# Kernel optimization log

Hardware: AMD Instinct MI355X
Metric: run time of the kernel (lower is better)

The kernel has to match this reference:

```python
import jax, jax.numpy as jnp
import numpy as np

B, M, Wc, K, IN = 32, 65536, 64, 8, 512
R = K + 1                      # sparse_reads + last_used slot
IFACE = 2 * Wc + R + 1         # interface_size = 2w + r + 1


def setup_inputs() -> dict:
    key = jax.random.key(0)
    ks = jax.random.split(key, 8)
    xi = jax.random.normal(ks[0], (B, IN), jnp.float32)
    sparse = jax.random.normal(ks[1], (B, M, Wc), jnp.float32)
    read_weights = jax.random.uniform(ks[2], (B, 1, R), jnp.float32)
    read_vectors = jax.random.normal(ks[3], (B, R, Wc), jnp.float32)
    W = jax.random.normal(ks[4], (IN, IFACE), jnp.float32) / np.sqrt(IN).astype(np.float32)
    b = jnp.zeros((IFACE,), jnp.float32)
    read_positions = jax.random.randint(ks[5], (B, R), 0, M, dtype=jnp.int32)
    last_used_mem = jax.random.randint(ks[6], (B,), 0, M, dtype=jnp.int32)
    return dict(xi=xi, sparse=sparse, read_weights=read_weights,
                read_vectors=read_vectors, W=W, b=b,
                read_positions=read_positions, last_used_mem=last_used_mem)


def reference(xi, sparse, read_weights, read_vectors, W, b, read_positions, last_used_mem):
    bsz = xi.shape[0]
    w, r, m, k = Wc, R, M, K
    # interface linear (independent_linears=False path)
    iface = xi @ W + b                                   # [b, 2w+r+1]
    read_query = iface[:, :w]                            # [b, w]
    write_vector = iface[:, w:2 * w][:, None, :]         # [b, 1, w]
    ig = iface[:, 2 * w:2 * w + r][:, None, :]           # [b, 1, r]
    write_gate = jax.nn.sigmoid(iface[:, -1])[:, None, None]  # [b, 1, 1]
    # write(): interpolate read weights, rank-1 update of read_vectors
    ww = write_gate * (ig * read_weights + (1.0 - ig))   # [b, 1, r]
    rv = read_vectors + jnp.einsum('bor,bow->brw', ww, write_vector)  # [b, r, w]
    # write_into_memory(): for l in range(b): sparse[:, positions[l], :] = rv
    flat_pos = read_positions.reshape(-1)                # [b*r]
    flat_k = jnp.tile(jnp.arange(r, dtype=jnp.int32), bsz)
    order = jnp.full((m,), -1, jnp.int32).at[flat_pos].max(
        jnp.arange(bsz * r, dtype=jnp.int32))            # last writer per slot
    k_final = flat_k[order[flat_pos]]                    # winning k per written entry
    sparse = sparse.at[:, flat_pos, :].set(rv[:, k_final, :])
    # read_from_sparse_memory(): brute-force exact KNN (squared L2, replaces FLANN kd-tree)
    d = (jnp.sum(sparse * sparse, -1)
         - 2.0 * jnp.einsum('bmw,bw->bm', sparse, read_query)
         + jnp.sum(read_query * read_query, -1, keepdims=True))  # [b, m]
    neg_d, pos = jax.lax.top_k(-d, k)                    # k nearest
    dist = -neg_d                                        # [b, k]
    pos = jnp.concatenate([pos.astype(jnp.int32), last_used_mem[:, None]], axis=1)  # [b, r]
    dist = jnp.concatenate([dist, jnp.zeros((bsz, 1), dist.dtype)], axis=1)          # [b, r]
    dist = dist / jnp.max(dist, axis=1, keepdims=True)   # distances / max(distances)
    gathered = jnp.take_along_axis(sparse, pos[:, :, None], axis=1)  # [b, r, w]
    read_weights_new = dist[:, None, :]                  # [b, 1, r]
    return gathered[:, :k, :], read_weights_new, gathered
```

## Files before the change

### kernel.cpp

```cpp
#include <hip/hip_runtime.h>
#include <float.h>
#include <math.h>

#define Bz    32
#define Mz    65536
#define WCz   64
#define Rz    9
#define INz   512
#define IFz   138
#define NBLK  64
#define RPB   1024


__device__ __forceinline__ bool pless(float d1, int i1, float d2, int i2) {
    return (d1 < d2) || (d1 == d2 && i1 < i2);
}

__global__ __launch_bounds__(256) void k_iface(
    const float* __restrict__ xi, const float* __restrict__ W,
    const float* __restrict__ bias, float* __restrict__ iface)
{
    int o = blockIdx.x * 256 + threadIdx.x;
    if (o >= Bz * IFz) return;
    int b = o / IFz, j = o % IFz;
    const float* x = xi + b * INz;
    float a0 = 0.f, a1 = 0.f, a2 = 0.f, a3 = 0.f;
    #pragma unroll 4
    for (int i = 0; i < INz; i += 4) {
        a0 = fmaf(x[i + 0], W[(i + 0) * IFz + j], a0);
        a1 = fmaf(x[i + 1], W[(i + 1) * IFz + j], a1);
        a2 = fmaf(x[i + 2], W[(i + 2) * IFz + j], a2);
        a3 = fmaf(x[i + 3], W[(i + 3) * IFz + j], a3);
    }
    iface[o] = (a0 + a1) + (a2 + a3) + bias[j];
}

__global__ __launch_bounds__(256) void k_prep(
    const float* __restrict__ iface,
    const float* __restrict__ read_weights,
    const float* __restrict__ read_vectors,
    const int*   __restrict__ read_positions,
    float* __restrict__ ws_q, float* __restrict__ ws_qq,
    float* __restrict__ ws_rv, float* __restrict__ ws_dv,
    int* __restrict__ ws_wpos, int* __restrict__ ws_wk, int* __restrict__ ws_nw)
{
    __shared__ float ww_s[Bz * Rz];
    __shared__ int nw_s;
    int t = threadIdx.x;
    if (t == 0) nw_s = 0;

    for (int i = t; i < Bz * WCz; i += 256) {
        int b = i >> 6, w = i & 63;
        ws_q[i] = iface[b * IFz + w];
    }
    for (int i = t; i < Bz * Rz; i += 256) {
        int b = i / Rz, r = i % Rz;
        float x    = iface[b * IFz + (IFz - 1)];
        float gate = 1.0f / (1.0f + expf(-x));
        float ig   = iface[b * IFz + 2 * WCz + r];
        float rw   = read_weights[i];
        ww_s[i] = gate * (ig * rw + (1.0f - ig));
    }
    __syncthreads();

    if (t < Bz) {
        float s = 0.f;
        for (int w = 0; w < WCz; w++) { float v = ws_q[t * WCz + w]; s = fmaf(v, v, s); }
        ws_qq[t] = s;
    }
    for (int i = t; i < Bz * Rz * WCz; i += 256) {
        int br = i >> 6, w = i & 63;
        int b  = br / Rz;
        ws_rv[i] = fmaf(ww_s[br], iface[b * IFz + WCz + w], read_vectors[i]);
    }
    for (int i = t; i < Bz * Rz; i += 256) {
        int p = read_positions[i];
        bool win = true;
        for (int j = i + 1; j < Bz * Rz; j++)
            if (read_positions[j] == p) { win = false; break; }
        if (win) {
            int slot = atomicAdd(&nw_s, 1);
            ws_wpos[slot] = p;
            ws_wk[slot]   = i % Rz;
        }
    }
    __syncthreads();

    for (int i = t; i < Bz * Rz; i += 256) {
        int b = i / Rz;
        const float* rv = ws_rv + i * WCz;
        const float* q  = ws_q + b * WCz;
        float s1 = 0.f, s2 = 0.f;
        for (int w = 0; w < WCz; w++) {
            float v = rv[w];
            s1 = fmaf(v, v, s1);
            s2 = fmaf(v, q[w], s2);
        }
        ws_dv[i] = s1 - 2.0f * s2 + ws_qq[b];
    }
    if (t == 0) ws_nw[0] = nw_s;
}

__global__ __launch_bounds__(256) void k_dist(
    const float* __restrict__ sparse,
    const float* __restrict__ ws_q, const float* __restrict__ ws_qq,
    const int* __restrict__ ws_wpos, const int* __restrict__ ws_nw,
    float* __restrict__ cand_d, int* __restrict__ cand_i)
{
    __shared__ float d_s[RPB];
    __shared__ unsigned int bmp[RPB / 32];
    __shared__ float md[64 * 8];
    __shared__ int   mi[64 * 8];

    int t = threadIdx.x;
    int b = blockIdx.y;
    int chunk = blockIdx.x;
    int lo = chunk * RPB;

    if (t < RPB / 32) bmp[t] = 0u;
    __syncthreads();
    int nw = ws_nw[0];
    for (int i = t; i < nw; i += 256) {
        int rel = ws_wpos[i] - lo;
        if ((unsigned)rel < (unsigned)RPB) atomicOr(&bmp[rel >> 5], 1u << (rel & 31));
    }

    int e = t & 15;
    int g = t >> 4;
    const float4 q4 = *(const float4*)(ws_q + b * WCz + e * 4);
    float m0 = -2.f * q4.x, m1 = -2.f * q4.y, m2 = -2.f * q4.z, m3 = -2.f * q4.w;
    float qq = ws_qq[b];
    const float* base = sparse + ((size_t)b * Mz + lo) * WCz + e * 4;
    __syncthreads();

    #pragma unroll 1
    for (int it = 0; it < RPB / 16; it += 4) {
        float4 f[4];
        int rl[4];
        #pragma unroll
        for (int u = 0; u < 4; u++) {
            rl[u] = (it + u) * 16 + g;
            f[u] = *(const float4*)(base + (size_t)rl[u] * WCz);
        }
        #pragma unroll
        for (int u = 0; u < 4; u++) {
            float p = f[u].x * (f[u].x + m0);
            p = fmaf(f[u].y, f[u].y + m1, p);
            p = fmaf(f[u].z, f[u].z + m2, p);
            p = fmaf(f[u].w, f[u].w + m3, p);
            p += __shfl_xor(p, 1);
            p += __shfl_xor(p, 2);
            p += __shfl_xor(p, 4);
            p += __shfl_xor(p, 8);
            if (e == 0) {
                float d = p + qq;
                int r = rl[u];
                if ((bmp[r >> 5] >> (r & 31)) & 1u) d = FLT_MAX;
                d_s[r] = d;
            }
        }
    }
    __syncthreads();

    if (t < 64) {
        float ld[8]; int li[8];
        #pragma unroll
        for (int k = 0; k < 8; k++) { ld[k] = FLT_MAX; li[k] = 0x7FFFFFFF; }
        for (int r = t; r < RPB; r += 64) {
            float v = d_s[r];
            int idx = lo + r;
            if (pless(v, idx, ld[7], li[7])) {
                #pragma unroll
                for (int k = 7; k >= 0; k--) {
                    bool ltp = (k > 0) && pless(v, idx, ld[k - 1], li[k - 1]);
                    bool lth = pless(v, idx, ld[k], li[k]);
                    if (lth) {
                        if (ltp) { ld[k] = ld[k - 1]; li[k] = li[k - 1]; }
                        else     { ld[k] = v;         li[k] = idx; }
                    }
                }
            }
        }
        #pragma unroll
        for (int k = 0; k < 8; k++) { md[t * 8 + k] = ld[k]; mi[t * 8 + k] = li[k]; }
    }
    __syncthreads();
    for (int step = 32; step >= 1; step >>= 1) {
        if (t < step) {
            float od[8]; int oi[8];
            int ia = 0, ib = 0;
            #pragma unroll
            for (int k = 0; k < 8; k++) {
                float da = md[t * 8 + ia],        db = md[(t + step) * 8 + ib];
                int   ja = mi[t * 8 + ia],        jb = mi[(t + step) * 8 + ib];
                if (pless(da, ja, db, jb)) { od[k] = da; oi[k] = ja; ia++; }
                else                       { od[k] = db; oi[k] = jb; ib++; }
            }
            #pragma unroll
            for (int k = 0; k < 8; k++) { md[t * 8 + k] = od[k]; mi[t * 8 + k] = oi[k]; }
        }
        __syncthreads();
    }
    if (t < 8) {
        cand_d[((size_t)b * NBLK + chunk) * 8 + t] = md[t];
        cand_i[((size_t)b * NBLK + chunk) * 8 + t] = mi[t];
    }
}

__global__ __launch_bounds__(256) void k_final(
    const float* __restrict__ sparse,
    const int* __restrict__ last_used,
    const float* __restrict__ ws_rv, const float* __restrict__ ws_dv,
    const int* __restrict__ ws_wpos, const int* __restrict__ ws_wk,
    const int* __restrict__ ws_nw,
    const float* __restrict__ cand_d, const int* __restrict__ cand_i,
    float* __restrict__ out)
{
    __shared__ float cd[1024]; __shared__ int ci[1024];
    __shared__ float md[64 * 8]; __shared__ int mi[64 * 8];
    __shared__ int pos_s[Rz]; __shared__ float dist_s[Rz]; __shared__ int fk_s[Rz];

    int t = threadIdx.x;
    int b = blockIdx.x;
    int nw = ws_nw[0];

    for (int i = t; i < NBLK * 8; i += 256) {
        cd[i] = cand_d[(size_t)b * NBLK * 8 + i];
        ci[i] = cand_i[(size_t)b * NBLK * 8 + i];
    }
    for (int i = t; i < nw; i += 256) {
        cd[NBLK * 8 + i] = ws_dv[b * Rz + ws_wk[i]];
        ci[NBLK * 8 + i] = ws_wpos[i];
    }
    for (int i = NBLK * 8 + nw + t; i < 1024; i += 256) { cd[i] = FLT_MAX; ci[i] = 0x7FFFFFFF; }
    __syncthreads();

    if (t < 64) {
        float ld[8]; int li[8];
        #pragma unroll
        for (int k = 0; k < 8; k++) { ld[k] = FLT_MAX; li[k] = 0x7FFFFFFF; }
        for (int r = t; r < 1024; r += 64) {
            float v = cd[r]; int idx = ci[r];
            if (pless(v, idx, ld[7], li[7])) {
                #pragma unroll
                for (int k = 7; k >= 0; k--) {
                    bool ltp = (k > 0) && pless(v, idx, ld[k - 1], li[k - 1]);
                    bool lth = pless(v, idx, ld[k], li[k]);
                    if (lth) {
                        if (ltp) { ld[k] = ld[k - 1]; li[k] = li[k - 1]; }
                        else     { ld[k] = v;         li[k] = idx; }
                    }
                }
            }
        }
        #pragma unroll
        for (int k = 0; k < 8; k++) { md[t * 8 + k] = ld[k]; mi[t * 8 + k] = li[k]; }
    }
    __syncthreads();
    for (int step = 32; step >= 1; step >>= 1) {
        if (t < step) {
            float od[8]; int oi[8];
            int ia = 0, ib = 0;
            #pragma unroll
            for (int k = 0; k < 8; k++) {
                float da = md[t * 8 + ia],        db = md[(t + step) * 8 + ib];
                int   ja = mi[t * 8 + ia],        jb = mi[(t + step) * 8 + ib];
                if (pless(da, ja, db, jb)) { od[k] = da; oi[k] = ja; ia++; }
                else                       { od[k] = db; oi[k] = jb; ib++; }
            }
            #pragma unroll
            for (int k = 0; k < 8; k++) { md[t * 8 + k] = od[k]; mi[t * 8 + k] = oi[k]; }
        }
        __syncthreads();
    }

    if (t == 0) {
        float norm = 0.f;
        for (int j = 0; j < 8; j++) { dist_s[j] = md[j]; pos_s[j] = mi[j]; norm = fmaxf(norm, md[j]); }
        dist_s[8] = 0.f;
        pos_s[8]  = last_used[b];
        for (int j = 0; j < Rz; j++)
            out[Bz * 8 * WCz + b * Rz + j] = dist_s[j] / norm;
    }
    __syncthreads();

    if (t < Rz) {
        int p = pos_s[t]; int fk = -1;
        for (int i = 0; i < nw; i++)
            if (ws_wpos[i] == p) { fk = ws_wk[i]; break; }
        fk_s[t] = fk;
    }
    __syncthreads();

    for (int i = t; i < Rz * WCz; i += 256) {
        int j = i >> 6, w = i & 63;
        int p = pos_s[j]; int fk = fk_s[j];
        float v = (fk >= 0) ? ws_rv[(b * Rz + fk) * WCz + w]
                            : sparse[((size_t)b * Mz + p) * WCz + w];
        out[Bz * 8 * WCz + Bz * Rz + (b * Rz + j) * WCz + w] = v;
        if (j < 8) out[(b * 8 + j) * WCz + w] = v;
    }
}

extern "C" void kernel_launch(void* const* d_in, const int* in_sizes, int n_in,
                              void* d_out, int out_size, void* d_ws, size_t ws_size,
                              hipStream_t stream) {
    const float* xi             = (const float*)d_in[0];
    const float* sparse         = (const float*)d_in[1];
    const float* read_weights   = (const float*)d_in[2];
    const float* read_vectors   = (const float*)d_in[3];
    const float* W              = (const float*)d_in[4];
    const float* bias           = (const float*)d_in[5];
    const int*   read_positions = (const int*)d_in[6];
    const int*   last_used      = (const int*)d_in[7];
    float* out = (float*)d_out;
    float* ws  = (float*)d_ws;

    float* iface   = ws + 0;
    float* ws_q    = ws + 4416;
    float* ws_qq   = ws + 6464;
    float* ws_rv   = ws + 6496;
    float* ws_dv   = ws + 24928;
    int*   ws_wpos = (int*)(ws + 25216);
    int*   ws_wk   = (int*)(ws + 25504);
    int*   ws_nw   = (int*)(ws + 25792);
    float* cand_d  = ws + 25796;
    int*   cand_i  = (int*)(ws + 42180);

    k_iface<<<dim3((Bz * IFz + 255) / 256), dim3(256), 0, stream>>>(xi, W, bias, iface);
    k_prep<<<dim3(1), dim3(256), 0, stream>>>(iface, read_weights, read_vectors,
                                              read_positions, ws_q, ws_qq, ws_rv,
                                              ws_dv, ws_wpos, ws_wk, ws_nw);
    k_dist<<<dim3(NBLK, Bz), dim3(256), 0, stream>>>(sparse, ws_q, ws_qq, ws_wpos,
                                                     ws_nw, cand_d, cand_i);
    k_final<<<dim3(Bz), dim3(256), 0, stream>>>(sparse, last_used, ws_rv, ws_dv,
                                                ws_wpos, ws_wk, ws_nw, cand_d,
                                                cand_i, out);
}
```

Measured before the change: 809.1 us.

## Fuse interface linear into per-batch prep kernel and deepen distance loads

Merges the interface matmul kernel into the prep kernel, which now launches one block per batch instead of a single block, so the serial prep work is spread across blocks and one launch is removed. The distance kernel now builds its written-slot bitmap straight from read_positions, dropping its dependence on the deduplicated write list. It also issues eight float4 loads per iteration instead of four to keep more memory requests in flight. Risks are higher register pressure in the distance loop and the deduplication still running serially in block 0.

```diff
diff --git a/kernel.cpp b/kernel.cpp
--- a/kernel.cpp
+++ b/kernel.cpp
@@ -16,27 +16,9 @@
     return (d1 < d2) || (d1 == d2 && i1 < i2);
 }
 
-__global__ __launch_bounds__(256) void k_iface(
+__global__ __launch_bounds__(256) void k_prep(
     const float* __restrict__ xi, const float* __restrict__ W,
-    const float* __restrict__ bias, float* __restrict__ iface)
-{
-    int o = blockIdx.x * 256 + threadIdx.x;
-    if (o >= Bz * IFz) return;
-    int b = o / IFz, j = o % IFz;
-    const float* x = xi + b * INz;
-    float a0 = 0.f, a1 = 0.f, a2 = 0.f, a3 = 0.f;
-    #pragma unroll 4
-    for (int i = 0; i < INz; i += 4) {
-        a0 = fmaf(x[i + 0], W[(i + 0) * IFz + j], a0);
-        a1 = fmaf(x[i + 1], W[(i + 1) * IFz + j], a1);
-        a2 = fmaf(x[i + 2], W[(i + 2) * IFz + j], a2);
-        a3 = fmaf(x[i + 3], W[(i + 3) * IFz + j], a3);
-    }
-    iface[o] = (a0 + a1) + (a2 + a3) + bias[j];
-}
-
-__global__ __launch_bounds__(256) void k_prep(
-    const float* __restrict__ iface,
+    const float* __restrict__ bias,
     const float* __restrict__ read_weights,
     const float* __restrict__ read_vectors,
     const int*   __restrict__ read_positions,
@@ -44,67 +26,87 @@
     float* __restrict__ ws_rv, float* __restrict__ ws_dv,
     int* __restrict__ ws_wpos, int* __restrict__ ws_wk, int* __restrict__ ws_nw)
 {
-    __shared__ float ww_s[Bz * Rz];
-    __shared__ int nw_s;
-    int t = threadIdx.x;
+    __shared__ float xs[INz];
+    __shared__ float if_s[IFz];
+    __shared__ float ww_s[Rz];
+    __shared__ float rv_s[Rz * WCz];
+    __shared__ float qq_s;
+    __shared__ int   pos_s[Bz * Rz];
+    __shared__ int   nw_s;
+
+    int t = threadIdx.x, b = blockIdx.x;
+    for (int i = t; i < INz / 4; i += 256)
+        ((float4*)xs)[i] = ((const float4*)(xi + (size_t)b * INz))[i];
+    for (int i = t; i < Bz * Rz; i += 256) pos_s[i] = read_positions[i];
     if (t == 0) nw_s = 0;
-
-    for (int i = t; i < Bz * WCz; i += 256) {
-        int b = i >> 6, w = i & 63;
-        ws_q[i] = iface[b * IFz + w];
-    }
-    for (int i = t; i < Bz * Rz; i += 256) {
-        int b = i / Rz, r = i % Rz;
-        float x    = iface[b * IFz + (IFz - 1)];
-        float gate = 1.0f / (1.0f + expf(-x));
-        float ig   = iface[b * IFz + 2 * WCz + r];
-        float rw   = read_weights[i];
-        ww_s[i] = gate * (ig * rw + (1.0f - ig));
-    }
-    __syncthreads();
-
-    if (t < Bz) {
-        float s = 0.f;
-        for (int w = 0; w < WCz; w++) { float v = ws_q[t * WCz + w]; s = fmaf(v, v, s); }
-        ws_qq[t] = s;
-    }
-    for (int i = t; i < Bz * Rz * WCz; i += 256) {
-        int br = i >> 6, w = i & 63;
-        int b  = br / Rz;
-        ws_rv[i] = fmaf(ww_s[br], iface[b * IFz + WCz + w], read_vectors[i]);
-    }
-    for (int i = t; i < Bz * Rz; i += 256) {
-        int p = read_positions[i];
-        bool win = true;
-        for (int j = i + 1; j < Bz * Rz; j++)
-            if (read_positions[j] == p) { win = false; break; }
-        if (win) {
-            int slot = atomicAdd(&nw_s, 1);
-            ws_wpos[slot] = p;
-            ws_wk[slot]   = i % Rz;
-        }
-    }
-    __syncthreads();
-
-    for (int i = t; i < Bz * Rz; i += 256) {
-        int b = i / Rz;
-        const float* rv = ws_rv + i * WCz;
-        const float* q  = ws_q + b * WCz;
+    __syncthreads();
+
+    if (t < IFz) {
+        float a0 = 0.f, a1 = 0.f, a2 = 0.f, a3 = 0.f;
+        #pragma unroll 4
+        for (int i = 0; i < INz; i += 4) {
+            a0 = fmaf(xs[i + 0], W[(i + 0) * IFz + t], a0);
+            a1 = fmaf(xs[i + 1], W[(i + 1) * IFz + t], a1);
+            a2 = fmaf(xs[i + 2], W[(i + 2) * IFz + t], a2);
+            a3 = fmaf(xs[i + 3], W[(i + 3) * IFz + t], a3);
+        }
+        if_s[t] = (a0 + a1) + (a2 + a3) + bias[t];
+    }
+    __syncthreads();
+
+    if (t < 64) {
+        float v = if_s[t];
+        ws_q[b * WCz + t] = v;
+        float p = v * v;
+        p += __shfl_xor(p, 1);  p += __shfl_xor(p, 2);  p += __shfl_xor(p, 4);
+        p += __shfl_xor(p, 8);  p += __shfl_xor(p, 16); p += __shfl_xor(p, 32);
+        if (t == 0) { qq_s = p; ws_qq[b] = p; }
+    } else if (t < 64 + Rz) {
+        int r = t - 64;
+        float g  = 1.0f / (1.0f + expf(-if_s[IFz - 1]));
+        float ig = if_s[2 * WCz + r];
+        ww_s[r] = g * (ig * read_weights[b * Rz + r] + (1.0f - ig));
+    }
+    __syncthreads();
+
+    for (int i = t; i < Rz * WCz; i += 256) {
+        int r = i >> 6, w = i & 63;
+        float v = fmaf(ww_s[r], if_s[WCz + w], read_vectors[(size_t)b * Rz * WCz + i]);
+        rv_s[i] = v;
+        ws_rv[(size_t)b * Rz * WCz + i] = v;
+    }
+
+    if (b == 0) {
+        for (int i = t; i < Bz * Rz; i += 256) {
+            int p = pos_s[i];
+            bool win = true;
+            for (int j = i + 1; j < Bz * Rz; j++)
+                if (pos_s[j] == p) { win = false; break; }
+            if (win) {
+                int slot = atomicAdd(&nw_s, 1);
+                ws_wpos[slot] = p;
+                ws_wk[slot]   = i % Rz;
+            }
+        }
+    }
+    __syncthreads();
+
+    if (t < Rz) {
         float s1 = 0.f, s2 = 0.f;
         for (int w = 0; w < WCz; w++) {
-            float v = rv[w];
+            float v = rv_s[t * WCz + w];
             s1 = fmaf(v, v, s1);
-            s2 = fmaf(v, q[w], s2);
-        }
-        ws_dv[i] = s1 - 2.0f * s2 + ws_qq[b];
-    }
-    if (t == 0) ws_nw[0] = nw_s;
+            s2 = fmaf(v, if_s[w], s2);
+        }
+        ws_dv[b * Rz + t] = s1 - 2.0f * s2 + qq_s;
+    }
+    if (b == 0 && t == 0) ws_nw[0] = nw_s;
 }
 
 __global__ __launch_bounds__(256) void k_dist(
     const float* __restrict__ sparse,
     const float* __restrict__ ws_q, const float* __restrict__ ws_qq,
-    const int* __restrict__ ws_wpos, const int* __restrict__ ws_nw,
+    const int* __restrict__ read_positions,
     float* __restrict__ cand_d, int* __restrict__ cand_i)
 {
     __shared__ float d_s[RPB];
@@ -119,9 +121,8 @@
 
     if (t < RPB / 32) bmp[t] = 0u;
     __syncthreads();
-    int nw = ws_nw[0];
-    for (int i = t; i < nw; i += 256) {
-        int rel = ws_wpos[i] - lo;
+    for (int i = t; i < Bz * Rz; i += 256) {
+        int rel = read_positions[i] - lo;
         if ((unsigned)rel < (unsigned)RPB) atomicOr(&bmp[rel >> 5], 1u << (rel & 31));
     }
 
@@ -134,16 +135,16 @@
     __syncthreads();
 
     #pragma unroll 1
-    for (int it = 0; it < RPB / 16; it += 4) {
-        float4 f[4];
-        int rl[4];
-        #pragma unroll
-        for (int u = 0; u < 4; u++) {
+    for (int it = 0; it < RPB / 16; it += 8) {
+        float4 f[8];
+        int rl[8];
+        #pragma unroll
+        for (int u = 0; u < 8; u++) {
             rl[u] = (it + u) * 16 + g;
             f[u] = *(const float4*)(base + (size_t)rl[u] * WCz);
         }
         #pragma unroll
-        for (int u = 0; u < 4; u++) {
+        for (int u = 0; u < 8; u++) {
             float p = f[u].x * (f[u].x + m0);
             p = fmaf(f[u].y, f[u].y + m1, p);
             p = fmaf(f[u].z, f[u].z + m2, p);
@@ -316,7 +317,6 @@
     float* out = (float*)d_out;
     float* ws  = (float*)d_ws;
 
-    float* iface   = ws + 0;
     float* ws_q    = ws + 4416;
     float* ws_qq   = ws + 6464;
     float* ws_rv   = ws + 6496;
@@ -327,12 +327,12 @@
     float* cand_d  = ws + 25796;
     int*   cand_i  = (int*)(ws + 42180);
 
-    k_iface<<<dim3((Bz * IFz + 255) / 256), dim3(256), 0, stream>>>(xi, W, bias, iface);
-    k_prep<<<dim3(1), dim3(256), 0, stream>>>(iface, read_weights, read_vectors,
-                                              read_positions, ws_q, ws_qq, ws_rv,
-                                              ws_dv, ws_wpos, ws_wk, ws_nw);
-    k_dist<<<dim3(NBLK, Bz), dim3(256), 0, stream>>>(sparse, ws_q, ws_qq, ws_wpos,
-                                                     ws_nw, cand_d, cand_i);
+    k_prep<<<dim3(Bz), dim3(256), 0, stream>>>(xi, W, bias, read_weights,
+                                               read_vectors, read_positions,
+                                               ws_q, ws_qq, ws_rv, ws_dv,
+                                               ws_wpos, ws_wk, ws_nw);
+    k_dist<<<dim3(NBLK, Bz), dim3(256), 0, stream>>>(sparse, ws_q, ws_qq,
+                                                     read_positions, cand_d, cand_i);
     k_final<<<dim3(Bz), dim3(256), 0, stream>>>(sparse, last_used, ws_rv, ws_dv,
                                                 ws_wpos, ws_wk, ws_nw, cand_d,
                                                 cand_i, out);
```

After: 783.6 us. -3.2%, faster.
